# Kernel tuning notes

Hardware: AMD Instinct MI355X
Metric: run time of the kernel (lower is better)

Reference implementation:

```python
import jax, jax.numpy as jnp
import numpy as np

L, H, C, V, B, T, Q = 6, 8, 512, 32000, 2, 4096, 256
N = C // H
LN_EPS = 1e-5
GN_EPS = 1e-5 * 64  # matches nn.GroupNorm(n_head, C, eps=1e-05*64)


def _shift(x):
    # ZeroPad2d((0,0,1,-1)): x[t] -> x[t-1], zero at t=0
    return jnp.concatenate([jnp.zeros_like(x[:, :1]), x[:, :-1]], axis=1)


def _layernorm(x, w):
    mu = x.mean(-1, keepdims=True)
    var = jnp.var(x, axis=-1, keepdims=True)
    return (x - mu) * jax.lax.rsqrt(var + LN_EPS) * w


def _time_mix(x, maa_k, maa_v, maa_r, maa_g, tdecay, tfaaaa, Wr, Wk, Wv, Wg, Wo, gn_w, gn_b):
    Bsz, Tlen, Cd = x.shape
    xx = _shift(x) - x
    xk = x + xx * maa_k
    xv = x + xx * maa_v
    xr = x + xx * maa_r
    xg = x + xx * maa_g
    r = (xr @ Wr.T).reshape(Bsz, Tlen, H, N).transpose(0, 2, 1, 3)   # B H T N
    k = (xk @ Wk.T).reshape(Bsz, Tlen, H, N).transpose(0, 2, 3, 1)   # B H N T
    v = (xv @ Wv.T).reshape(Bsz, Tlen, H, N).transpose(0, 2, 1, 3)   # B H T N
    g = jax.nn.silu(xg @ Wg.T)
    wdec = jnp.exp(-jnp.exp(tdecay))            # [H], per-head decay in (0,1)
    u = tfaaaa                                  # [H], 'first token' bonus
    ws = (wdec ** Q)[None, :, None, None]       # state decay across a chunk
    jj = jnp.arange(Q)
    wkv = (wdec[:, None] ** (Q - 1 - jj))[None, :, None, :]  # [1,H,1,Q]
    wb = (wdec[:, None] ** jj)[None, :, :, None]              # [1,H,Q,1]
    d = jj[:, None] - jj[None, :]                              # i - j
    # intra-chunk decay matrix: W[i,j] = u (i==j), wdec^(i-j-1) (i>j), 0 (i<j)
    Wmat = jnp.where(d > 0, wdec[:, None, None] ** jnp.maximum(d - 1, 0), 0.0)
    Wmat = (Wmat + u[:, None, None] * jnp.eye(Q, dtype=x.dtype))[None]  # [1,H,Q,Q]
    nc = Tlen // Q
    rc = r.reshape(Bsz, H, nc, Q, N).transpose(2, 0, 1, 3, 4)  # [nc,B,H,Q,N]
    kc = k.reshape(Bsz, H, N, nc, Q).transpose(3, 0, 1, 2, 4)  # [nc,B,H,N,Q]
    vc = v.reshape(Bsz, H, nc, Q, N).transpose(2, 0, 1, 3, 4)  # [nc,B,H,Q,N]

    def step(state, inp):
        rr, kk, vv = inp
        y = ((rr @ kk) * Wmat) @ vv + (rr @ state) * wb
        new_state = ws * state + (kk * wkv) @ vv
        return new_state, y

    state0 = jnp.zeros((Bsz, H, N, N), dtype=x.dtype)
    _, yc = jax.lax.scan(step, state0, (rc, kc, vc))
    y = yc.transpose(1, 2, 0, 3, 4).reshape(Bsz, H, Tlen, N).transpose(0, 2, 1, 3)  # B T H N
    # GroupNorm(n_head groups) == per (b,t,h) normalization over head dim N
    mu = y.mean(-1, keepdims=True)
    var = jnp.var(y, axis=-1, keepdims=True)
    y = (y - mu) * jax.lax.rsqrt(var + GN_EPS)
    y = y.reshape(Bsz, Tlen, Cd) * gn_w + gn_b
    return (y * g) @ Wo.T


def _channel_mix(x, cmaa_k, cmaa_r, Wck, Wcv, Wcr):
    xx = _shift(x) - x
    xk = x + xx * cmaa_k
    xr = x + xx * cmaa_r
    h = jnp.square(jax.nn.relu(xk @ Wck.T))
    h = h @ Wcv.T
    return jax.nn.sigmoid(xr @ Wcr.T) * h


def _forward(idx, wte, wpe, ln1_w, ln2_w, lnf_w, maa_k, maa_v, maa_r, maa_g, tdecay, tfaaaa,
             Wr, Wk, Wv, Wg, Wo, gn_w, gn_b, cmaa_k, cmaa_r, Wck, Wcv, Wcr):
    t = idx.shape[1]
    x = wte[idx] + wpe[:t]
    for l in range(L):
        x = x + _time_mix(_layernorm(x, ln1_w[l]), maa_k[l], maa_v[l], maa_r[l], maa_g[l],
                          tdecay[l], tfaaaa[l], Wr[l], Wk[l], Wv[l], Wg[l], Wo[l], gn_w[l], gn_b[l])
        x = x + _channel_mix(_layernorm(x, ln2_w[l]), cmaa_k[l], cmaa_r[l], Wck[l], Wcv[l], Wcr[l])
    x = _layernorm(x, lnf_w)
    logits = x[:, -1:, :] @ wte.T  # targets=None path: only last position
    return logits


def setup_inputs() -> dict:
    key = jax.random.key(0)
    ks = jax.random.split(key, 12)
    idx = jax.random.randint(ks[0], (B, T), 0, V)
    # structured per-layer init tensors (exact formulas from __init__)
    ddd = np.arange(C, dtype=np.float32) / C
    hh = np.arange(H, dtype=np.float32) / (H - 1)
    maa_k = np.zeros((L, C), np.float32); maa_v = np.zeros((L, C), np.float32)
    maa_r = np.zeros((L, C), np.float32); maa_g = np.zeros((L, C), np.float32)
    tdecay = np.zeros((L, H), np.float32); tfaaaa = np.zeros((L, H), np.float32)
    cmaa_k = np.zeros((L, C), np.float32); cmaa_r = np.zeros((L, C), np.float32)
    for l in range(L):
        r0 = l / max(L - 1, 1)
        r1 = 1.0 - l / L
        maa_k[l] = 1.0 - ddd ** r1
        maa_v[l] = 1.0 - (ddd ** r1 + 0.3 * r0)
        maa_r[l] = 1.0 - ddd ** (0.5 * r1)
        maa_g[l] = 1.0 - ddd ** (0.5 * r1)
        tdecay[l] = -6.0 + 5.0 * hh ** (0.7 + 1.3 * r0)
        tfaaaa[l] = r0 * (1.0 - hh)
        cmaa_k[l] = 1.0 - ddd ** r1
        cmaa_r[l] = 1.0 - ddd ** r1
    s = 0.02
    return {
        'idx': idx,
        'wte': jax.random.normal(ks[1], (V, C), jnp.float32) * s,
        'wpe': jax.random.normal(ks[2], (T, C), jnp.float32) * s,
        'ln1_w': jnp.ones((L, C), jnp.float32),
        'ln2_w': jnp.ones((L, C), jnp.float32),
        'lnf_w': jnp.ones((C,), jnp.float32),
        'maa_k': jnp.asarray(maa_k), 'maa_v': jnp.asarray(maa_v),
        'maa_r': jnp.asarray(maa_r), 'maa_g': jnp.asarray(maa_g),
        'tdecay': jnp.asarray(tdecay), 'tfaaaa': jnp.asarray(tfaaaa),
        'Wr': jax.random.normal(ks[3], (L, C, C), jnp.float32) * s,
        'Wk': jax.random.normal(ks[4], (L, C, C), jnp.float32) * s,
        'Wv': jax.random.normal(ks[5], (L, C, C), jnp.float32) * s,
        'Wg': jax.random.normal(ks[6], (L, C, C), jnp.float32) * s,
        'Wo': jax.random.normal(ks[7], (L, C, C), jnp.float32) * (s / np.sqrt(2 * L)),
        'gn_w': jnp.ones((L, C), jnp.float32),
        'gn_b': jnp.zeros((L, C), jnp.float32),
        'cmaa_k': jnp.asarray(cmaa_k), 'cmaa_r': jnp.asarray(cmaa_r),
        'Wck': jax.random.normal(ks[8], (L, 3 * C, C), jnp.float32) * s,
        'Wcv': jax.random.normal(ks[9], (L, C, 3 * C), jnp.float32) * s,
        'Wcr': jax.random.normal(ks[10], (L, C, C), jnp.float32) * s,
    }


def reference(idx, wte, wpe, ln1_w, ln2_w, lnf_w, maa_k, maa_v, maa_r, maa_g, tdecay, tfaaaa,
              Wr, Wk, Wv, Wg, Wo, gn_w, gn_b, cmaa_k, cmaa_r, Wck, Wcv, Wcr):
    return _forward(idx, wte, wpe, ln1_w, ln2_w, lnf_w, maa_k, maa_v, maa_r, maa_g, tdecay,
                    tfaaaa, Wr, Wk, Wv, Wg, Wo, gn_w, gn_b, cmaa_k, cmaa_r, Wck, Wcv, Wcr)
```

## Files before the change

kernel.cpp:

```cpp
#include <hip/hip_runtime.h>

#define L_ 6
#define H_ 8
#define C_ 512
#define V_ 32000
#define B_ 2
#define T_ 4096
#define Q_ 256
#define N_ 64
#define NC_ 16
#define M_ 8192

typedef unsigned short u16;
typedef __attribute__((ext_vector_type(8))) short bf16x8;
typedef __attribute__((ext_vector_type(4))) float f32x4;

__device__ __forceinline__ float bf2f(u16 u){
  return __uint_as_float(((unsigned int)u) << 16);
}
__device__ __forceinline__ u16 f2bf(float f){
  unsigned int x = __float_as_uint(f);
  return (u16)((x + 0x7fffu + ((x >> 16) & 1u)) >> 16);
}

__device__ __forceinline__ void gl_lds16(const u16* g, u16* l){
  __builtin_amdgcn_global_load_lds((const __attribute__((address_space(1))) void*)g,
                                   (__attribute__((address_space(3))) void*)l, 16, 0, 0);
}

__global__ __launch_bounds__(256) void detect_kernel(const void* __restrict__ probe,
                                                     int* __restrict__ flag){
  __shared__ int cnt;
  if (threadIdx.x == 0) cnt = 0;
  __syncthreads();
  const u16* p = (const u16*)probe;
  int c = 0;
  for (int i = threadIdx.x; i < 2048; i += 256){
    int e = (p[i] >> 7) & 0xFF;
    if (e >= 128) c++;
  }
  atomicAdd(&cnt, c);
  __syncthreads();
  if (threadIdx.x == 0) *flag = (cnt > 32) ? 1 : 0;
}

struct PtrTab { const void* raw[23]; long long off[23]; };

__global__ __launch_bounds__(64) void fill_ptab(PtrTab pt, const u16* __restrict__ pool,
    const int* __restrict__ flag, const u16** __restrict__ ptab){
  int i = threadIdx.x;
  if (i < 23)
    ptab[i+1] = (*flag) ? (pool + pt.off[i]) : (const u16*)pt.raw[i];
}

struct CvtTab { const void* s[21]; int off8[22]; int bstart[22]; };

__global__ __launch_bounds__(256) void convert_all(CvtTab t, u16* __restrict__ pool,
                                                   const int* __restrict__ flag){
  if (!*flag) return;
  int i = 0;
  #pragma unroll
  for (int k = 1; k < 21; k++) if ((int)blockIdx.x >= t.bstart[k]) i = k;
  const void* sp = t.s[0];
  #pragma unroll
  for (int k = 1; k < 21; k++) if (i == k) sp = t.s[k];
  const int n8 = t.off8[i+1] - t.off8[i];
  const int nb = t.bstart[i+1] - t.bstart[i];
  const int lb = (int)blockIdx.x - t.bstart[i];
  uint4* dp = (uint4*)pool + t.off8[i];
  const int stride = nb * 256;
  const float4* sf = (const float4*)sp;
  for (int j = lb*256 + (int)threadIdx.x; j < n8; j += stride){
    float4 a0 = sf[2*j], a1 = sf[2*j+1];
    uint4 r0;
    r0.x = (unsigned)f2bf(a0.x) | ((unsigned)f2bf(a0.y) << 16);
    r0.y = (unsigned)f2bf(a0.z) | ((unsigned)f2bf(a0.w) << 16);
    r0.z = (unsigned)f2bf(a1.x) | ((unsigned)f2bf(a1.y) << 16);
    r0.w = (unsigned)f2bf(a1.z) | ((unsigned)f2bf(a1.w) << 16);
    dp[j] = r0;
  }
}

__global__ __launch_bounds__(256) void embed_kernel(const int* __restrict__ idx,
    const void* __restrict__ wteR, const void* __restrict__ wpeR,
    const int* __restrict__ flag, float* __restrict__ x){
  int row = blockIdx.x;
  int t = row & (T_-1);
  int tok = idx[row];
  float* xo = x + (size_t)row * C_;
  int c = threadIdx.x;
  float a0,a1,b0,b1;
  if (*flag){
    const float* we = (const float*)wteR + (size_t)tok * C_;
    const float* wp = (const float*)wpeR + (size_t)t * C_;
    a0 = we[c]; a1 = we[c+256]; b0 = wp[c]; b1 = wp[c+256];
  } else {
    const u16* we = (const u16*)wteR + (size_t)tok * C_;
    const u16* wp = (const u16*)wpeR + (size_t)t * C_;
    a0 = bf2f(we[c]); a1 = bf2f(we[c+256]); b0 = bf2f(wp[c]); b1 = bf2f(wp[c+256]);
  }
  xo[c]     = a0 + b0;
  xo[c+256] = a1 + b1;
}

__global__ __launch_bounds__(256) void ln_tmix_kernel(const float* __restrict__ x,
    const u16* const* __restrict__ ptab, int l,
    u16* __restrict__ xk, u16* __restrict__ xv, u16* __restrict__ xr, u16* __restrict__ xg){
  const u16* w  = ptab[3] + l*C_;
  const u16* mk = ptab[6] + l*C_;
  const u16* mv = ptab[7] + l*C_;
  const u16* mr = ptab[8] + l*C_;
  const u16* mg = ptab[9] + l*C_;
  int row = blockIdx.x; int t = row & (T_-1);
  size_t off = (size_t)row*C_;
  const float* cur = x + off;
  int c = threadIdx.x;
  float v0 = cur[c], v1 = cur[c+256];
  float p0 = 0.f, p1 = 0.f;
  if (t){ p0 = cur[c - C_]; p1 = cur[c+256 - C_]; }
  float s = v0+v1, ss = v0*v0+v1*v1;
  float sp = p0+p1, ssp = p0*p0+p1*p1;
  int lane = c & 63, wid = c >> 6;
  #pragma unroll
  for (int o=32;o>0;o>>=1){
    s  += __shfl_down(s,o,64);  ss  += __shfl_down(ss,o,64);
    sp += __shfl_down(sp,o,64); ssp += __shfl_down(ssp,o,64);
  }
  __shared__ float r1[4], r2[4], r3[4], r4[4];
  if (lane==0){ r1[wid]=s; r2[wid]=ss; r3[wid]=sp; r4[wid]=ssp; }
  __syncthreads();
  if (c==0){
    float a =r1[0]+r1[1]+r1[2]+r1[3], bq=r2[0]+r2[1]+r2[2]+r2[3];
    float ap=r3[0]+r3[1]+r3[2]+r3[3], bp=r4[0]+r4[1]+r4[2]+r4[3];
    float mu  = a *(1.f/C_); float var  = bq*(1.f/C_) - mu*mu;
    float mup = ap*(1.f/C_); float varp = bp*(1.f/C_) - mup*mup;
    r1[0]=mu;  r2[0]=rsqrtf(fmaxf(var ,0.f)+1e-5f);
    r3[0]=mup; r4[0]=rsqrtf(fmaxf(varp,0.f)+1e-5f);
  }
  __syncthreads();
  float mu=r1[0], inv=r2[0], mup=r3[0], invp=r4[0];
  #pragma unroll
  for (int p=0;p<2;p++){
    int cc = c + p*256;
    float wc = bf2f(w[cc]);
    float xc = ((p?v1:v0)-mu)*inv*wc;
    float xp = t ? ((p?p1:p0)-mup)*invp*wc : 0.f;
    float xx = xp - xc;
    xk[off+cc] = f2bf(xc + xx*bf2f(mk[cc]));
    xv[off+cc] = f2bf(xc + xx*bf2f(mv[cc]));
    xr[off+cc] = f2bf(xc + xx*bf2f(mr[cc]));
    xg[off+cc] = f2bf(xc + xx*bf2f(mg[cc]));
  }
}

__global__ __launch_bounds__(256) void ln_cmix_kernel(const float* __restrict__ x,
    const u16* const* __restrict__ ptab, int l,
    u16* __restrict__ xk, u16* __restrict__ xr){
  const u16* w  = ptab[4]  + l*C_;
  const u16* mk = ptab[19] + l*C_;
  const u16* mr = ptab[20] + l*C_;
  int row = blockIdx.x; int t = row & (T_-1);
  size_t off = (size_t)row*C_;
  const float* cur = x + off;
  int c = threadIdx.x;
  float v0 = cur[c], v1 = cur[c+256];
  float p0 = 0.f, p1 = 0.f;
  if (t){ p0 = cur[c - C_]; p1 = cur[c+256 - C_]; }
  float s = v0+v1, ss = v0*v0+v1*v1;
  float sp = p0+p1, ssp = p0*p0+p1*p1;
  int lane = c & 63, wid = c >> 6;
  #pragma unroll
  for (int o=32;o>0;o>>=1){
    s  += __shfl_down(s,o,64);  ss  += __shfl_down(ss,o,64);
    sp += __shfl_down(sp,o,64); ssp += __shfl_down(ssp,o,64);
  }
  __shared__ float r1[4], r2[4], r3[4], r4[4];
  if (lane==0){ r1[wid]=s; r2[wid]=ss; r3[wid]=sp; r4[wid]=ssp; }
  __syncthreads();
  if (c==0){
    float a =r1[0]+r1[1]+r1[2]+r1[3], bq=r2[0]+r2[1]+r2[2]+r2[3];
    float ap=r3[0]+r3[1]+r3[2]+r3[3], bp=r4[0]+r4[1]+r4[2]+r4[3];
    float mu  = a *(1.f/C_); float var  = bq*(1.f/C_) - mu*mu;
    float mup = ap*(1.f/C_); float varp = bp*(1.f/C_) - mup*mup;
    r1[0]=mu;  r2[0]=rsqrtf(fmaxf(var ,0.f)+1e-5f);
    r3[0]=mup; r4[0]=rsqrtf(fmaxf(varp,0.f)+1e-5f);
  }
  __syncthreads();
  float mu=r1[0], inv=r2[0], mup=r3[0], invp=r4[0];
  #pragma unroll
  for (int p=0;p<2;p++){
    int cc = c + p*256;
    float wc = bf2f(w[cc]);
    float xc = ((p?v1:v0)-mu)*inv*wc;
    float xp = t ? ((p?p1:p0)-mup)*invp*wc : 0.f;
    float xx = xp - xc;
    xk[off+cc] = f2bf(xc + xx*bf2f(mk[cc]));
    xr[off+cc] = f2bf(xc + xx*bf2f(mr[cc]));
  }
}

__global__ __launch_bounds__(256) void lnf_last(const float* __restrict__ x,
    const u16* const* __restrict__ ptab, float* __restrict__ xf){
  const u16* w = ptab[5];
  int b = blockIdx.x;
  const float* xr = x + ((size_t)b*T_ + (T_-1))*C_;
  int c = threadIdx.x;
  float v0 = xr[c], v1 = xr[c+256];
  float s = v0+v1, ss = v0*v0+v1*v1;
  int lane = c & 63, wid = c >> 6;
  #pragma unroll
  for (int o=32;o>0;o>>=1){ s += __shfl_down(s,o,64); ss += __shfl_down(ss,o,64); }
  __shared__ float r1[4], r2[4];
  if (lane==0){ r1[wid]=s; r2[wid]=ss; }
  __syncthreads();
  if (c==0){
    float a=r1[0]+r1[1]+r1[2]+r1[3], bq=r2[0]+r2[1]+r2[2]+r2[3];
    float mu = a*(1.f/C_);
    float var = bq*(1.f/C_) - mu*mu;
    r1[0]=mu; r2[0]=rsqrtf(fmaxf(var,0.f)+1e-5f);
  }
  __syncthreads();
  float mu=r1[0], inv=r2[0];
  xf[b*C_+c]     = (v0-mu)*inv*bf2f(w[c]);
  xf[b*C_+c+256] = (v1-mu)*inv*bf2f(w[c+256]);
}

#define ACT_RELU2_BF16 1
#define ACT_ADD_F32 2
#define ACT_BF16 3
#define ACT_CMIX 4
#define ACT_SIG_BF16 7

template<int ACT>
__device__ __forceinline__ void gemm_mfma_body(u16* __restrict__ Al, u16* __restrict__ Bl,
    const u16* __restrict__ X, const u16* __restrict__ W,
    float* __restrict__ Yf, u16* __restrict__ Yb, const u16* __restrict__ AuxB,
    int Ndim, int Kdim, int bm, int bn){
  const int tid = threadIdx.x;
  const int wv = tid >> 6, ln = tid & 63;
  const int m16 = ln & 15, q = ln >> 4;

  f32x4 acc[2][4];
  #pragma unroll
  for (int i=0;i<2;i++)
    #pragma unroll
    for (int j=0;j<4;j++) acc[i][j] = f32x4{0.f,0.f,0.f,0.f};

  const int r0 = wv*8 + (ln >> 3);
  const int c0 = (ln & 7)*8;
  const u16* ga = X + (size_t)(bm + r0)*Kdim + c0;
  const u16* gb = W + (size_t)(bn + r0)*Kdim + c0;
  u16* la = Al + r0*64 + c0;
  u16* lb = Bl + r0*64 + c0;

  for (int k0=0; k0<Kdim; k0+=64){
    #pragma unroll
    for (int s=0;s<4;s++)
      gl_lds16(ga + (size_t)(s*32)*Kdim + k0, la + s*2048);
    #pragma unroll
    for (int s=0;s<2;s++)
      gl_lds16(gb + (size_t)(s*32)*Kdim + k0, lb + s*2048);
    __syncthreads();
    #pragma unroll
    for (int kh=0; kh<2; kh++){
      bf16x8 af[2], bfr[4];
      #pragma unroll
      for (int i=0;i<2;i++) af[i]  = *(const bf16x8*)(Al + (wv*32 + i*16 + m16)*64 + kh*32 + q*8);
      #pragma unroll
      for (int j=0;j<4;j++) bfr[j] = *(const bf16x8*)(Bl + (j*16 + m16)*64 + kh*32 + q*8);
      #pragma unroll
      for (int i=0;i<2;i++)
        #pragma unroll
        for (int j=0;j<4;j++)
          acc[i][j] = __builtin_amdgcn_mfma_f32_16x16x32_bf16(af[i], bfr[j], acc[i][j], 0, 0, 0);
    }
    __syncthreads();
  }

  #pragma unroll
  for (int i=0;i<2;i++){
    int row = bm + wv*32 + i*16 + q*4;
    #pragma unroll
    for (int j=0;j<4;j++){
      int col = bn + j*16 + m16;
      #pragma unroll
      for (int r=0;r<4;r++){
        size_t off = (size_t)(row + r)*Ndim + col;
        float v = acc[i][j][r];
        if (ACT==ACT_ADD_F32) Yf[off] += v;
        else if (ACT==ACT_CMIX){ Yf[off] += v * bf2f(AuxB[off]); }
        else if (ACT==ACT_BF16) Yb[off] = f2bf(v);
        else if (ACT==ACT_RELU2_BF16){ float rr = v>0.f ? v : 0.f; Yb[off] = f2bf(rr*rr); }
        else if (ACT==ACT_SIG_BF16) Yb[off] = f2bf(1.f/(1.f+expf(-v)));
      }
    }
  }
}

#define GEMM_SH __shared__ __align__(16) u16 SH[128*64 + 64*64]

__global__ __launch_bounds__(256,4) void gemm4_mfma(const u16* const* __restrict__ ptab, int l,
    const u16* __restrict__ Abase,
    u16* __restrict__ Rb, u16* __restrict__ Kb, u16* __restrict__ Vb, u16* __restrict__ Gb){
  GEMM_SH;
  const size_t MC = (size_t)M_*C_;
  const size_t ws = (size_t)l*C_*C_;
  const int bm = blockIdx.x*128, bn = blockIdx.y*64;
  switch (blockIdx.z){
    case 0:  gemm_mfma_body<ACT_BF16>(SH, SH+128*64, Abase + 2*MC, ptab[12]+ws, nullptr, Rb, nullptr, C_, C_, bm, bn); break;
    case 1:  gemm_mfma_body<ACT_BF16>(SH, SH+128*64, Abase,        ptab[13]+ws, nullptr, Kb, nullptr, C_, C_, bm, bn); break;
    case 2:  gemm_mfma_body<ACT_BF16>(SH, SH+128*64, Abase + 1*MC, ptab[14]+ws, nullptr, Vb, nullptr, C_, C_, bm, bn); break;
    default: gemm_mfma_body<ACT_BF16>(SH, SH+128*64, Abase + 3*MC, ptab[15]+ws, nullptr, Gb, nullptr, C_, C_, bm, bn); break;
  }
}

__global__ __launch_bounds__(256,4) void gemm_ck_cr(const u16* const* __restrict__ ptab, int l,
    const u16* __restrict__ MK, u16* __restrict__ H1,
    const u16* __restrict__ MV, u16* __restrict__ RRb){
  GEMM_SH;
  if (blockIdx.y < 24)
    gemm_mfma_body<ACT_RELU2_BF16>(SH, SH+128*64, MK, ptab[21]+(size_t)l*3*C_*C_, nullptr, H1, nullptr,
                                   3*C_, C_, blockIdx.x*128, blockIdx.y*64);
  else
    gemm_mfma_body<ACT_SIG_BF16>(SH, SH+128*64, MV, ptab[23]+(size_t)l*C_*C_, nullptr, RRb, nullptr,
                                 C_, C_, blockIdx.x*128, (blockIdx.y-24)*64);
}

__global__ __launch_bounds__(256,4) void gemm_wo(const u16* const* __restrict__ ptab, int l,
    const u16* __restrict__ YGN, float* __restrict__ X){
  GEMM_SH;
  gemm_mfma_body<ACT_ADD_F32>(SH, SH+128*64, YGN, ptab[16]+(size_t)l*C_*C_, X, nullptr, nullptr,
                              C_, C_, blockIdx.x*128, blockIdx.y*64);
}

__global__ __launch_bounds__(256,4) void gemm_cmix(const u16* const* __restrict__ ptab, int l,
    const u16* __restrict__ H1, float* __restrict__ X, const u16* __restrict__ RRb){
  GEMM_SH;
  gemm_mfma_body<ACT_CMIX>(SH, SH+128*64, H1, ptab[22]+(size_t)l*3*C_*C_, X, nullptr, RRb,
                           C_, 3*C_, blockIdx.x*128, blockIdx.y*64);
}

__global__ __launch_bounds__(256) void kvtrans(const u16* __restrict__ Kb, const u16* __restrict__ Vb,
    u16* __restrict__ Kt, u16* __restrict__ Vt, const u16* const* __restrict__ ptab, int l){
  __shared__ __align__(16) u16 tile[64*64];
  const int t0 = blockIdx.x*64, bh = blockIdx.y, b = bh>>3, h = bh&7;
  const bool isK = (blockIdx.z == 1);
  const u16* src = isK ? Kb : Vb;
  u16* dst = isK ? Kt : Vt;
  float l2w = 0.f;
  if (isK){
    const u16* td = ptab[10] + l*H_;
    l2w = -expf(bf2f(td[h])) * 1.44269504f;
  }
  const int tid = threadIdx.x;
  #pragma unroll
  for (int it=0; it<2; ++it){
    int tl = it*32 + (tid>>3);
    int n0 = (tid&7)*8;
    union {uint4 q; u16 e[8];} v;
    v.q = *(const uint4*)(src + ((size_t)(b*T_ + t0 + tl))*C_ + h*N_ + n0);
    if (isK){
      int tloc = (t0 + tl) & (Q_-1);
      float sc = exp2f(l2w * (float)(Q_-1 - tloc));
      #pragma unroll
      for (int e=0;e<8;++e) v.e[e] = f2bf(bf2f(v.e[e])*sc);
    }
    int col = n0 ^ (((tl>>3)&7)<<3);
    *(uint4*)&tile[tl*64 + col] = v.q;
  }
  __syncthreads();
  #pragma unroll
  for (int it=0; it<2; ++it){
    int nl = it*32 + (tid>>3);
    int t0l = (tid&7)*8;
    int swz = (tid&7)<<3;
    union {uint4 q; u16 h2[8];} pk;
    #pragma unroll
    for (int e=0;e<8;++e)
      pk.h2[e] = tile[(t0l+e)*64 + (nl ^ swz)];
    *(uint4*)(dst + ((size_t)(bh*N_ + nl))*T_ + t0 + t0l) = pk.q;
  }
}

__global__ __launch_bounds__(256) void wkv_state_mfma(const u16* __restrict__ Kt,
    const u16* __restrict__ Vt, float* __restrict__ S){
  const int c = blockIdx.x, bh = blockIdx.y;
  const int tid = threadIdx.x, wv = tid >> 6, ln = tid & 63;
  const int m16 = ln & 15, q = ln >> 4;
  const u16* ka = Kt + (size_t)(bh*N_ + wv*16 + m16)*T_ + c*Q_;
  const u16* vb = Vt + (size_t)(bh*N_ + m16)*T_ + c*Q_;
  f32x4 acc[4];
  #pragma unroll
  for (int nt=0;nt<4;++nt) acc[nt] = f32x4{0.f,0.f,0.f,0.f};
  #pragma unroll
  for (int ks=0; ks<8; ++ks){
    bf16x8 af = *(const bf16x8*)(ka + ks*32 + q*8);
    #pragma unroll
    for (int nt=0;nt<4;++nt){
      bf16x8 bv = *(const bf16x8*)(vb + (size_t)(nt*16)*T_ + ks*32 + q*8);
      acc[nt] = __builtin_amdgcn_mfma_f32_16x16x32_bf16(af, bv, acc[nt], 0,0,0);
    }
  }
  float* Sp = S + ((size_t)bh*NC_ + c)*(N_*N_);
  #pragma unroll
  for (int nt=0;nt<4;++nt)
    #pragma unroll
    for (int r=0;r<4;++r)
      Sp[(wv*16 + q*4 + r)*N_ + nt*16 + m16] = acc[nt][r];
}

__global__ __launch_bounds__(256) void wkv_prefix(float* __restrict__ S,
    const u16* const* __restrict__ ptab, int l){
  const int bh = blockIdx.x, h = bh&7;
  const u16* td = ptab[10] + l*H_;
  const float l2w = -expf(bf2f(td[h])) * 1.44269504f;
  const float wsd = exp2f(l2w * (float)Q_);
  float* Sp = S + (size_t)bh*NC_*N_*N_;
  for (int e=threadIdx.x; e<N_*N_; e+=256){
    float cur = 0.f;
    for (int cc=0;cc<NC_;++cc){
      float sc = Sp[(size_t)cc*N_*N_ + e];
      Sp[(size_t)cc*N_*N_ + e] = cur;
      cur = wsd*cur + sc;
    }
  }
}

__global__ __launch_bounds__(256) void wkv_fused(const u16* __restrict__ Rb,
    const u16* __restrict__ Kb, const u16* __restrict__ Vt, const float* __restrict__ S,
    const u16* const* __restrict__ ptab, int l,
    const u16* __restrict__ g, u16* __restrict__ out){
  __shared__ float wpow[Q_];
  __shared__ float st[64][68];
  __shared__ float rs[64][68];
  __shared__ __align__(16) float ylds[64][68];
  u16 (*P)[16][72] = reinterpret_cast<u16(*)[16][72]>(&ylds[0][0]);
  const u16* td  = ptab[10] + l*H_;
  const u16* tf  = ptab[11] + l*H_;
  const u16* gnw = ptab[17] + l*C_;
  const u16* gnb = ptab[18] + l*C_;
  const int c = blockIdx.x>>2, ip = blockIdx.x&3;
  const int bh = blockIdx.y, b = bh>>3, h = bh&7;
  const int tid = threadIdx.x, wv = tid >> 6, ln = tid & 63;
  const int m16 = ln & 15, q = ln >> 4;
  const int tx = tid&15, ty = tid>>4;
  const float l2w = -expf(bf2f(td[h])) * 1.44269504f;
  const float uu = bf2f(tf[h]);
  wpow[tid] = exp2f(l2w * (float)tid);
  const float* Sp = S + ((size_t)bh*NC_ + c)*(N_*N_);
  for (int e=tid;e<N_*N_;e+=256) st[e>>6][e&63] = Sp[e];
  const size_t base = ((size_t)b*T_ + (size_t)c*Q_)*C_ + h*N_;
  const int i0 = ip*64;
  {
    const int rrr = tid >> 6, cc2 = tid & 63;
    for (int it=0;it<16;++it){ int i=it*4+rrr; rs[i][cc2]=bf2f(Rb[base+(size_t)(i0+i)*C_+cc2]); }
  }
  __syncthreads();
  const int iw0 = ip*64 + wv*16;
  const u16* rrow = Rb + base + (size_t)(iw0 + m16)*C_;
  bf16x8 af0 = *(const bf16x8*)(rrow + q*8);
  bf16x8 af1 = *(const bf16x8*)(rrow + 32 + q*8);
  f32x4 acc[4];
  #pragma unroll
  for (int nt=0;nt<4;++nt) acc[nt] = f32x4{0.f,0.f,0.f,0.f};
  const int irow = iw0 + q*4;
  const u16* vtb = Vt + (size_t)(bh*N_)*T_ + (size_t)c*Q_;
  for (int jt=0; jt<=ip; ++jt){
    f32x4 s[4];
    #pragma unroll
    for (int j2=0;j2<4;++j2) s[j2] = f32x4{0.f,0.f,0.f,0.f};
    #pragma unroll
    for (int j2=0;j2<4;++j2){
      const u16* kr = Kb + base + (size_t)(jt*64 + j2*16 + m16)*C_;
      bf16x8 b0 = *(const bf16x8*)(kr + q*8);
      bf16x8 b1 = *(const bf16x8*)(kr + 32 + q*8);
      s[j2] = __builtin_amdgcn_mfma_f32_16x16x32_bf16(af0, b0, s[j2], 0,0,0);
      s[j2] = __builtin_amdgcn_mfma_f32_16x16x32_bf16(af1, b1, s[j2], 0,0,0);
    }
    #pragma unroll
    for (int j2=0;j2<4;++j2){
      int jc = jt*64 + j2*16 + m16;
      #pragma unroll
      for (int r=0;r<4;++r){
        int ic = irow + r;
        float w = (jc < ic) ? wpow[ic-jc-1] : ((jc==ic) ? uu : 0.f);
        P[wv][q*4+r][j2*16+m16] = f2bf(s[j2][r]*w);
      }
    }
    __asm__ volatile("s_waitcnt lgkmcnt(0)" ::: "memory");
    #pragma unroll
    for (int kp=0;kp<2;++kp){
      bf16x8 ap = *(const bf16x8*)&P[wv][m16][kp*32 + q*8];
      #pragma unroll
      for (int nt=0;nt<4;++nt){
        bf16x8 bv = *(const bf16x8*)(vtb + (size_t)(nt*16 + m16)*T_ + jt*64 + kp*32 + q*8);
        acc[nt] = __builtin_amdgcn_mfma_f32_16x16x32_bf16(ap, bv, acc[nt], 0,0,0);
      }
    }
  }
  __syncthreads();
  #pragma unroll
  for (int nt=0;nt<4;++nt)
    #pragma unroll
    for (int r=0;r<4;++r)
      ylds[wv*16 + q*4 + r][nt*16 + m16] = acc[nt][r];
  __syncthreads();
  float acc2[4][4] = {};
  #pragma unroll
  for (int kk4=0;kk4<16;++kk4){
    f32x4 sv[4], rv[4];
    #pragma unroll
    for (int kkk=0;kkk<4;++kkk) sv[kkk] = *(const f32x4*)&st[kk4*4+kkk][tx*4];
    #pragma unroll
    for (int ii=0;ii<4;++ii)    rv[ii]  = *(const f32x4*)&rs[ty*4+ii][kk4*4];
    #pragma unroll
    for (int ii=0;ii<4;++ii)
      #pragma unroll
      for (int kkk=0;kkk<4;++kkk)
        #pragma unroll
        for (int nn=0;nn<4;++nn)
          acc2[ii][nn] += rv[ii][kkk]*sv[kkk][nn];
  }
  #pragma unroll
  for (int ii=0;ii<4;ii++){
    int tl = ty*4+ii;
    int il = i0 + tl;
    size_t roff = base + (size_t)il*C_;
    float w = wpow[il];
    f32x4 yv = *(const f32x4*)&ylds[tl][tx*4];
    float val[4];
    float s=0.f, ss=0.f;
    #pragma unroll
    for (int nn=0;nn<4;nn++){
      float v = yv[nn] + w*acc2[ii][nn];
      val[nn]=v; s+=v; ss+=v*v;
    }
    #pragma unroll
    for (int o=8;o>0;o>>=1){ s+=__shfl_xor(s,o,64); ss+=__shfl_xor(ss,o,64); }
    float mu = s*(1.f/N_);
    float var = ss*(1.f/N_) - mu*mu;
    float inv = rsqrtf(fmaxf(var,0.f) + 6.4e-4f);
    union { ushort4 v; u16 e[4]; } gv, ov;
    gv.v = *(const ushort4*)(g + roff + tx*4);
    #pragma unroll
    for (int nn=0;nn<4;nn++){
      int ci = h*N_ + tx*4 + nn;
      float gg = bf2f(gv.e[nn]);
      float sil = gg/(1.f+expf(-gg));
      ov.e[nn] = f2bf(((val[nn]-mu)*inv*bf2f(gnw[ci]) + bf2f(gnb[ci]))*sil);
    }
    *(ushort4*)(out + roff + tx*4) = ov.v;
  }
}

__global__ __launch_bounds__(256) void logits_kernel(const float* __restrict__ xf,
    const void* __restrict__ wteR, void* __restrict__ out, const int* __restrict__ flag){
  const int wid = threadIdx.x>>6, lane = threadIdx.x&63;
  const int gw = blockIdx.x*4 + wid;
  const int b = gw / V_, v = gw - b*V_;
  const float* xr = xf + b*C_;
  float s = 0.f;
  if (*flag){
    const float* wrow = (const float*)wteR + (size_t)v*C_;
    float4 w0 = ((const float4*)wrow)[lane*2];
    float4 w1 = ((const float4*)wrow)[lane*2+1];
    const float* xp = xr + lane*8;
    s = w0.x*xp[0] + w0.y*xp[1] + w0.z*xp[2] + w0.w*xp[3]
      + w1.x*xp[4] + w1.y*xp[5] + w1.z*xp[6] + w1.w*xp[7];
  } else {
    const u16* wrow = (const u16*)wteR + (size_t)v*C_;
    union {uint4 q; u16 h[8];} uu;
    uu.q = *(const uint4*)(wrow + lane*8);
    #pragma unroll
    for (int j=0;j<8;j++) s += bf2f(uu.h[j])*xr[lane*8+j];
  }
  #pragma unroll
  for (int o=32;o>0;o>>=1) s += __shfl_down(s,o,64);
  if (lane==0){
    size_t o = (size_t)b*V_ + v;
    if (*flag) ((float*)out)[o] = s;
    else       ((u16*)out)[o]   = f2bf(s);
  }
}

extern "C" void kernel_launch(void* const* d_in, const int* in_sizes, int n_in,
                              void* d_out, int out_size, void* d_ws, size_t ws_size,
                              hipStream_t stream){
  (void)out_size; (void)ws_size; (void)n_in;
  const int* idx  = (const int*)d_in[0];

  char* ws = (char*)d_ws;
  const size_t MC  = (size_t)M_*C_;
  size_t o = 0;
  int* flag = (int*)(ws + o);            o += 1024;
  const u16** ptab = (const u16**)(ws + o); o += 1024;
  float* X   = (float*)(ws + o);         o += MC*4;
  u16* MK = (u16*)(ws + o);              o += MC*2;
  u16* MV = (u16*)(ws + o);              o += MC*2;
  u16* MR = (u16*)(ws + o);              o += MC*2;
  u16* MG = (u16*)(ws + o);              o += MC*2;
  u16* Rb = (u16*)(ws + o);              o += MC*2;
  u16* Kb = (u16*)(ws + o);              o += MC*2;
  u16* Vb = (u16*)(ws + o);              o += MC*2;
  u16* Gb = (u16*)(ws + o);              o += MC*2;
  u16* Kt = (u16*)(ws + o);              o += MC*2;
  u16* Vt = (u16*)(ws + o);              o += MC*2;
  float* XF = (float*)(ws + o);          o += 65536;
  u16* pool = (u16*)(ws + o);
  u16* YGN = MK;
  float* S  = (float*)MR;
  u16* H1 = Rb;
  u16* RRb = MR;

  detect_kernel<<<1,256,0,stream>>>(d_in[12], flag);
  CvtTab tab; PtrTab pt;
  int nblocks;
  {
    size_t poff = 0; int acc8 = 0, bacc = 0;
    long long total8 = 0;
    for (int i=3;i<24;i++) total8 += (long long)(in_sizes[i] >> 3);
    pt.raw[0] = d_in[1]; pt.off[0] = 0;
    pt.raw[1] = d_in[2]; pt.off[1] = 0;
    for (int i=3;i<24;i++){
      int j = i-3;
      pt.raw[i-1] = d_in[i];
      pt.off[i-1] = (long long)poff;
      poff += (size_t)in_sizes[i];
      tab.s[j] = d_in[i];
      tab.off8[j] = acc8;
      tab.bstart[j] = bacc;
      int n8 = in_sizes[i] >> 3;
      int nb = (int)(((long long)n8 * 2048 + total8 - 1) / total8);
      if (nb < 1) nb = 1;
      acc8 += n8; bacc += nb;
    }
    tab.off8[21] = acc8; tab.bstart[21] = bacc;
    nblocks = bacc;
  }
  fill_ptab<<<1,64,0,stream>>>(pt, pool, flag, ptab);
  convert_all<<<nblocks,256,0,stream>>>(tab, pool, flag);

  embed_kernel<<<M_,256,0,stream>>>(idx, d_in[1], d_in[2], flag, X);
  dim3 g4 (M_/128, C_/64, 4);
  dim3 gkv(T_/64, B_*H_, 2);
  dim3 gck(M_/128, 32);
  dim3 gwo(M_/128, C_/64);
  for (int l=0;l<L_;++l){
    ln_tmix_kernel<<<M_,256,0,stream>>>(X, ptab, l, MK,MV,MR,MG);
    gemm4_mfma<<<g4,256,0,stream>>>(ptab, l, MK, Rb, Kb, Vb, Gb);
    kvtrans<<<gkv,256,0,stream>>>(Kb, Vb, Kt, Vt, ptab, l);
    wkv_state_mfma<<<dim3(NC_, B_*H_),256,0,stream>>>(Kt, Vt, S);
    wkv_prefix<<<B_*H_,256,0,stream>>>(S, ptab, l);
    wkv_fused<<<dim3(NC_*4, B_*H_),256,0,stream>>>(Rb, Kb, Vt, S, ptab, l, Gb, YGN);
    gemm_wo<<<gwo,256,0,stream>>>(ptab, l, YGN, X);
    ln_cmix_kernel<<<M_,256,0,stream>>>(X, ptab, l, MK, MV);
    gemm_ck_cr<<<gck,256,0,stream>>>(ptab, l, MK, H1, MV, RRb);
    gemm_cmix<<<gwo,256,0,stream>>>(ptab, l, H1, X, RRb);
  }
  lnf_last<<<B_,256,0,stream>>>(X, ptab, XF);
  logits_kernel<<<(B_*V_)/4,256,0,stream>>>(XF, d_in[1], d_out, flag);
}
```

Measured before the change: 1.553 ms.

## Compute inter-chunk state contribution with bf16 MFMA and fuse epilogue in registers

The r·state product in the fused WKV kernel moves from a scalar fp32 LDS-tiled loop to bf16 MFMA. The chunk state is stored transposed by the state kernel, converted to bf16 in shared memory, and multiplied using the R fragments already held in registers. The group-norm/gating epilogue now works directly on the MFMA accumulator layout, which removes the ylds staging buffer, the fp32 R reload and two barriers. In exchange, state precision drops to bf16 and the g loads and output stores become scalar 16-bit accesses instead of vectorised ones.

```diff
diff --git a/kernel.cpp b/kernel.cpp
--- a/kernel.cpp
+++ b/kernel.cpp
@@ -406,7 +406,7 @@
   for (int nt=0;nt<4;++nt)
     #pragma unroll
     for (int r=0;r<4;++r)
-      Sp[(wv*16 + q*4 + r)*N_ + nt*16 + m16] = acc[nt][r];
+      Sp[(nt*16 + m16)*N_ + (wv*16 + q*4 + r)] = acc[nt][r];
 }
 
 __global__ __launch_bounds__(256) void wkv_prefix(float* __restrict__ S,
@@ -431,10 +431,8 @@
     const u16* const* __restrict__ ptab, int l,
     const u16* __restrict__ g, u16* __restrict__ out){
   __shared__ float wpow[Q_];
-  __shared__ float st[64][68];
-  __shared__ float rs[64][68];
-  __shared__ __align__(16) float ylds[64][68];
-  u16 (*P)[16][72] = reinterpret_cast<u16(*)[16][72]>(&ylds[0][0]);
+  __shared__ __align__(16) u16 P[4][16][72];
+  __shared__ __align__(16) u16 stl[64][72];
   const u16* td  = ptab[10] + l*H_;
   const u16* tf  = ptab[11] + l*H_;
   const u16* gnw = ptab[17] + l*C_;
@@ -443,19 +441,19 @@
   const int bh = blockIdx.y, b = bh>>3, h = bh&7;
   const int tid = threadIdx.x, wv = tid >> 6, ln = tid & 63;
   const int m16 = ln & 15, q = ln >> 4;
-  const int tx = tid&15, ty = tid>>4;
   const float l2w = -expf(bf2f(td[h])) * 1.44269504f;
   const float uu = bf2f(tf[h]);
   wpow[tid] = exp2f(l2w * (float)tid);
-  const float* Sp = S + ((size_t)bh*NC_ + c)*(N_*N_);
-  for (int e=tid;e<N_*N_;e+=256) st[e>>6][e&63] = Sp[e];
+  {
+    const float* Sp = S + ((size_t)bh*NC_ + c)*(N_*N_);
+    #pragma unroll
+    for (int k2=0;k2<16;++k2){
+      int e = tid + k2*256;
+      stl[e>>6][e&63] = f2bf(Sp[e]);
+    }
+  }
+  __syncthreads();
   const size_t base = ((size_t)b*T_ + (size_t)c*Q_)*C_ + h*N_;
-  const int i0 = ip*64;
-  {
-    const int rrr = tid >> 6, cc2 = tid & 63;
-    for (int it=0;it<16;++it){ int i=it*4+rrr; rs[i][cc2]=bf2f(Rb[base+(size_t)(i0+i)*C_+cc2]); }
-  }
-  __syncthreads();
   const int iw0 = ip*64 + wv*16;
   const u16* rrow = Rb + base + (size_t)(iw0 + m16)*C_;
   bf16x8 af0 = *(const bf16x8*)(rrow + q*8);
@@ -498,58 +496,40 @@
       }
     }
   }
-  __syncthreads();
-  #pragma unroll
-  for (int nt=0;nt<4;++nt)
-    #pragma unroll
-    for (int r=0;r<4;++r)
-      ylds[wv*16 + q*4 + r][nt*16 + m16] = acc[nt][r];
-  __syncthreads();
-  float acc2[4][4] = {};
-  #pragma unroll
-  for (int kk4=0;kk4<16;++kk4){
-    f32x4 sv[4], rv[4];
-    #pragma unroll
-    for (int kkk=0;kkk<4;++kkk) sv[kkk] = *(const f32x4*)&st[kk4*4+kkk][tx*4];
-    #pragma unroll
-    for (int ii=0;ii<4;++ii)    rv[ii]  = *(const f32x4*)&rs[ty*4+ii][kk4*4];
-    #pragma unroll
-    for (int ii=0;ii<4;++ii)
-      #pragma unroll
-      for (int kkk=0;kkk<4;++kkk)
-        #pragma unroll
-        for (int nn=0;nn<4;++nn)
-          acc2[ii][nn] += rv[ii][kkk]*sv[kkk][nn];
-  }
-  #pragma unroll
-  for (int ii=0;ii<4;ii++){
-    int tl = ty*4+ii;
-    int il = i0 + tl;
+  f32x4 acc2[4];
+  #pragma unroll
+  for (int nt=0;nt<4;++nt) acc2[nt] = f32x4{0.f,0.f,0.f,0.f};
+  #pragma unroll
+  for (int nt=0;nt<4;++nt){
+    bf16x8 sb0 = *(const bf16x8*)&stl[nt*16 + m16][q*8];
+    bf16x8 sb1 = *(const bf16x8*)&stl[nt*16 + m16][32 + q*8];
+    acc2[nt] = __builtin_amdgcn_mfma_f32_16x16x32_bf16(af0, sb0, acc2[nt], 0,0,0);
+    acc2[nt] = __builtin_amdgcn_mfma_f32_16x16x32_bf16(af1, sb1, acc2[nt], 0,0,0);
+  }
+  #pragma unroll
+  for (int r=0;r<4;++r){
+    int il = irow + r;
     size_t roff = base + (size_t)il*C_;
     float w = wpow[il];
-    f32x4 yv = *(const f32x4*)&ylds[tl][tx*4];
     float val[4];
     float s=0.f, ss=0.f;
     #pragma unroll
-    for (int nn=0;nn<4;nn++){
-      float v = yv[nn] + w*acc2[ii][nn];
-      val[nn]=v; s+=v; ss+=v*v;
+    for (int nt=0;nt<4;++nt){
+      float v = acc[nt][r] + w*acc2[nt][r];
+      val[nt]=v; s+=v; ss+=v*v;
     }
     #pragma unroll
     for (int o=8;o>0;o>>=1){ s+=__shfl_xor(s,o,64); ss+=__shfl_xor(ss,o,64); }
     float mu = s*(1.f/N_);
     float var = ss*(1.f/N_) - mu*mu;
     float inv = rsqrtf(fmaxf(var,0.f) + 6.4e-4f);
-    union { ushort4 v; u16 e[4]; } gv, ov;
-    gv.v = *(const ushort4*)(g + roff + tx*4);
-    #pragma unroll
-    for (int nn=0;nn<4;nn++){
-      int ci = h*N_ + tx*4 + nn;
-      float gg = bf2f(gv.e[nn]);
+    #pragma unroll
+    for (int nt=0;nt<4;++nt){
+      int n = nt*16 + m16, ci = h*N_ + n;
+      float gg = bf2f(g[roff + n]);
       float sil = gg/(1.f+expf(-gg));
-      ov.e[nn] = f2bf(((val[nn]-mu)*inv*bf2f(gnw[ci]) + bf2f(gnb[ci]))*sil);
-    }
-    *(ushort4*)(out + roff + tx*4) = ov.v;
+      out[roff + n] = f2bf(((val[nt]-mu)*inv*bf2f(gnw[ci]) + bf2f(gnb[ci]))*sil);
+    }
   }
 }
 
```

After: 1.499 ms. -3.5%, faster.
